# Optimization experiments

Measured on AMD Instinct MI355X. Metric: run time of the kernel, lower is better.

## Reference

```python
import jax, jax.numpy as jnp
import numpy as np

N_NODES = 50000
N_EDGES = 800000
FEAT = 128
HID = 128
NUM_GRAPHS = 64
ODE_STEPS = 8   # fixed-step RK4 stand-in for adaptive odeint over CFG.ode_time_points
DEPTH = 1.0
EPS = 1e-5


def layer_norm(x, g, b):
    m = jnp.mean(x, axis=-1, keepdims=True)
    v = jnp.var(x, axis=-1, keepdims=True)
    return (x - m) * jax.lax.rsqrt(v + EPS) * g + b


def setup_inputs() -> dict:
    key = jax.random.key(0)
    ks = jax.random.split(key, 16)
    s = 1.0 / np.sqrt(FEAT)
    sh = 1.0 / np.sqrt(HID)
    inp = {
        "x": jax.random.normal(ks[0], (N_NODES, FEAT), jnp.float32),
        "edge_index": jax.random.randint(ks[1], (2, N_EDGES), 0, N_NODES, jnp.int64),
        "batch": jnp.sort(jax.random.randint(ks[2], (N_NODES,), 0, NUM_GRAPHS, jnp.int64)),
        "alpha": jnp.float32(0.8),
        "beta": jnp.float32(0.6),
        "phase": jnp.float32(0.7),
        "W_in": jax.random.normal(ks[3], (FEAT, HID), jnp.float32) * s,
        "b_in": jnp.zeros((HID,), jnp.float32),
        "g_in": jnp.ones((HID,), jnp.float32),
        "be_in": jnp.zeros((HID,), jnp.float32),
        "W_alt": jax.random.normal(ks[4], (FEAT, HID), jnp.float32) * s,
        "b_alt": jnp.zeros((HID,), jnp.float32),
        "g_alt": jnp.ones((HID,), jnp.float32),
        "be_alt": jnp.zeros((HID,), jnp.float32),
        "W_self": jax.random.normal(ks[5], (HID, HID), jnp.float32) * sh,
        "W_msg": jax.random.normal(ks[6], (HID, HID), jnp.float32) * sh,
        "b_ode": jnp.zeros((HID,), jnp.float32),
        "W_int": jax.random.normal(ks[7], (2 * HID, HID), jnp.float32) * sh / np.sqrt(2.0),
        "b_int": jnp.zeros((HID,), jnp.float32),
        "g_int": jnp.ones((HID,), jnp.float32),
        "be_int": jnp.zeros((HID,), jnp.float32),
        "W_out": jax.random.normal(ks[8], (HID, HID), jnp.float32) * sh,
        "b_out": jnp.zeros((HID,), jnp.float32),
    }
    return inp


def _forward(x, alpha, beta, phase,
             W_in, b_in, g_in, be_in,
             W_alt, b_alt, g_alt, be_alt,
             W_self, W_msg, b_ode,
             W_int, b_int, g_int, be_int,
             W_out, b_out,
             edge_index, batch):
    src, dst = edge_index[0], edge_index[1]
    # in-degree for mean aggregation (clamped to 1)
    deg = jax.ops.segment_sum(jnp.ones((src.shape[0],), jnp.float32), dst,
                              num_segments=N_NODES)
    deg = jnp.maximum(deg, 1.0)[:, None]

    # quantum amplitudes -> measurement probabilities (normalized)
    norm = jnp.sqrt(alpha ** 2 + beta ** 2)
    a, b = alpha / norm, beta / norm
    p0, p1 = a ** 2, b ** 2

    # two projection pathways in superposition
    h0 = jax.nn.gelu(layer_norm(x @ W_in + b_in, g_in, be_in))
    h1 = jax.nn.gelu(layer_norm(x @ W_alt + b_alt, g_alt, be_alt))
    h = jnp.sqrt(p0) * h0 + jnp.sqrt(p1) * h1  # [N, H]

    # Neural ODE: dh/dt = tanh(h W_self + mean_{j->i}(h_j W_msg) + b)
    def ode_f(h):
        msg = h[src] @ W_msg                       # [E, H] gather + GEMM
        agg = jax.ops.segment_sum(msg, dst, num_segments=N_NODES) / deg
        return jnp.tanh(h @ W_self + agg + b_ode)

    dt = jnp.float32(DEPTH / ODE_STEPS)

    def rk4_step(h, _):
        k1 = ode_f(h)
        k2 = ode_f(h + 0.5 * dt * k1)
        k3 = ode_f(h + 0.5 * dt * k2)
        k4 = ode_f(h + dt * k3)
        return h + (dt / 6.0) * (k1 + 2.0 * k2 + 2.0 * k3 + k4), None

    h, _ = jax.lax.scan(rk4_step, h, None, length=ODE_STEPS)

    # quantum interference mixing (conditional branch -> masked add)
    interf = 2.0 * jnp.sqrt(p0 * p1) * jnp.cos(phase)
    h_int = jnp.tanh(layer_norm(jnp.concatenate([h, h], axis=-1) @ W_int + b_int,
                                g_int, be_int))
    gate = jnp.where(jnp.abs(interf) > 0.01, interf, 0.0)
    h = h + gate * h_int

    # eval-mode collapse: if p1 >= p0, scale by Re(e^{i*phase}) = cos(phase)
    h = jnp.where(p0 > p1, h, h * jnp.cos(phase))

    h_out = h @ W_out + b_out

    # global mean pool over graphs
    cnt = jax.ops.segment_sum(jnp.ones((N_NODES,), jnp.float32), batch,
                              num_segments=NUM_GRAPHS)
    pooled = jax.ops.segment_sum(h_out, batch, num_segments=NUM_GRAPHS)
    return pooled / jnp.maximum(cnt, 1.0)[:, None]  # [NUM_GRAPHS, H]


def reference(x, edge_index, batch, alpha, beta, phase,
              W_in, b_in, g_in, be_in,
              W_alt, b_alt, g_alt, be_alt,
              W_self, W_msg, b_ode,
              W_int, b_int, g_int, be_int,
              W_out, b_out):
    return _forward(x, alpha, beta, phase,
                    W_in, b_in, g_in, be_in,
                    W_alt, b_alt, g_alt, be_alt,
                    W_self, W_msg, b_ode,
                    W_int, b_int, g_int, be_int,
                    W_out, b_out, edge_index, batch)
```

## Files before the change

kernel.cpp:

```cpp
#include <hip/hip_runtime.h>
#include <math.h>

#define NND 50000
#define NED 800000
#define HD  128
#define NG  64

typedef __attribute__((ext_vector_type(8))) short short8v;
typedef __attribute__((ext_vector_type(4))) float float4v;

__device__ __forceinline__ float gelu_t(float x) {
  const float c = 0.7978845608028654f;
  float t = tanhf(c * (x + 0.044715f * x * x * x));
  return 0.5f * x * (1.0f + t);
}

__device__ __forceinline__ unsigned short f2bf(float f) {
  unsigned int u = __float_as_uint(f);
  u += 0x7FFFu + ((u >> 16) & 1u);
  return (unsigned short)(u >> 16);
}
__device__ __forceinline__ float bf2f(unsigned short s) {
  return __uint_as_float(((unsigned int)s) << 16);
}
__device__ __forceinline__ float bflo(unsigned int u) { return __uint_as_float(u << 16); }
__device__ __forceinline__ float bfhi(unsigned int u) { return __uint_as_float(u & 0xFFFF0000u); }

__global__ void k_hist(const int* __restrict__ dst, int* __restrict__ degi) {
  int e = blockIdx.x * 256 + threadIdx.x;
  if (e < NED) atomicAdd(&degi[dst[e]], 1);
}

__global__ __launch_bounds__(1024) void k_scan(
    const int* __restrict__ degi, int* __restrict__ rowptr,
    int* __restrict__ cursor, float* __restrict__ deginv) {
  __shared__ int wsum[16];
  int tid = threadIdx.x;
  int lane = tid & 63;
  int wid = tid >> 6;
  int running = 0;
  for (int base = 0; base < NND; base += 1024) {
    int idx = base + tid;
    int v = (idx < NND) ? degi[idx] : 0;
    int s = v;
#pragma unroll
    for (int o = 1; o < 64; o <<= 1) {
      int t = __shfl_up(s, o, 64);
      if (lane >= o) s += t;
    }
    if (lane == 63) wsum[wid] = s;
    __syncthreads();
    if (wid == 0) {
      int ws = (lane < 16) ? wsum[lane] : 0;
#pragma unroll
      for (int o = 1; o < 16; o <<= 1) {
        int t = __shfl_up(ws, o, 64);
        if (lane >= o) ws += t;
      }
      if (lane < 16) wsum[lane] = ws;
    }
    __syncthreads();
    int woff = wid ? wsum[wid - 1] : 0;
    int excl = running + woff + s - v;
    if (idx < NND) {
      rowptr[idx] = excl;
      cursor[idx] = excl;
      deginv[idx] = 1.0f / (float)max(v, 1);
    }
    int tot = wsum[15];
    __syncthreads();
    running += tot;
  }
  if (tid == 0) rowptr[NND] = running;
}

__global__ void k_scatter(const int* __restrict__ src, const int* __restrict__ dst,
                          int* __restrict__ cursor, int* __restrict__ csrsrc) {
  int e = blockIdx.x * 256 + threadIdx.x;
  if (e < NED) {
    int d = dst[e];
    int pos = atomicAdd(&cursor[d], 1);
    csrsrc[pos] = src[e];
  }
}

__global__ void k_cnt(const int* __restrict__ batch, float* __restrict__ cnt) {
  int g = threadIdx.x;
  if (g >= NG) return;
  int lo, hi, ub_g, ub_gm1;
  lo = 0; hi = NND;
  while (lo < hi) { int mid = (lo + hi) >> 1; if (batch[mid] <= g) lo = mid + 1; else hi = mid; }
  ub_g = lo;
  if (g == 0) ub_gm1 = 0;
  else {
    lo = 0; hi = NND;
    int v = g - 1;
    while (lo < hi) { int mid = (lo + hi) >> 1; if (batch[mid] <= v) lo = mid + 1; else hi = mid; }
    ub_gm1 = lo;
  }
  cnt[g] = (float)(ub_g - ub_gm1);
}

__global__ void k_weff(const float* __restrict__ Wint, float* __restrict__ weff) {
  int i = blockIdx.x * 256 + threadIdx.x;
  if (i < HD * HD) weff[i] = Wint[i] + Wint[i + HD * HD];
}

__global__ void k_prepB(const float* __restrict__ Wself, const float* __restrict__ Wmsg,
                        unsigned short* __restrict__ Bt) {
  int i = blockIdx.x * 256 + threadIdx.x;
  if (i < 128 * 256) {
    int n = i >> 8, k = i & 255;
    float w = (k < HD) ? Wself[k * HD + n] : Wmsg[(k - HD) * HD + n];
    Bt[i] = f2bf(w);
  }
}

__global__ __launch_bounds__(256) void k_init(
    const float* __restrict__ x,
    const float* __restrict__ Win, const float* __restrict__ bin,
    const float* __restrict__ gin, const float* __restrict__ bein,
    const float* __restrict__ Walt, const float* __restrict__ balt,
    const float* __restrict__ galt, const float* __restrict__ bealt,
    const float* __restrict__ alphap, const float* __restrict__ betap,
    float* __restrict__ hdst, unsigned short* __restrict__ hbf)
{
  __shared__ float As[32][16];
  __shared__ float Bs[16][256];
  int tid = threadIdx.x;
  int lane = tid & 63;
  int ty = tid >> 6;
  int rowBase = blockIdx.x * 32;
  float acc[8][4];
#pragma unroll
  for (int i = 0; i < 8; ++i) { acc[i][0]=0.f; acc[i][1]=0.f; acc[i][2]=0.f; acc[i][3]=0.f; }

  for (int kc = 0; kc < 8; ++kc) {
    int k0 = kc * 16;
    if (tid < 128) {
      int r = tid >> 2, kq = (tid & 3) * 4;
      int row = rowBase + r; if (row >= NND) row = NND - 1;
      *(float4*)&As[r][kq] = *(const float4*)&x[(size_t)row * HD + k0 + kq];
    }
#pragma unroll
    for (int p = 0; p < 4; ++p) {
      int idx = p * 256 + tid;
      int kk = idx >> 6, cq = idx & 63;
      int col = cq * 4;
      int k = k0 + kk;
      const float* srcp = (col < HD) ? &Win[k * HD + col] : &Walt[k * HD + (col - HD)];
      *(float4*)&Bs[kk][col] = *(const float4*)srcp;
    }
    __syncthreads();
#pragma unroll
    for (int kq = 0; kq < 4; ++kq) {
      float4 b0 = *(float4*)&Bs[kq*4+0][lane*4];
      float4 b1 = *(float4*)&Bs[kq*4+1][lane*4];
      float4 b2 = *(float4*)&Bs[kq*4+2][lane*4];
      float4 b3 = *(float4*)&Bs[kq*4+3][lane*4];
#pragma unroll
      for (int i = 0; i < 8; ++i) {
        float4 a = *(float4*)&As[ty*8+i][kq*4];
        acc[i][0] = fmaf(a.x,b0.x,fmaf(a.y,b1.x,fmaf(a.z,b2.x,fmaf(a.w,b3.x,acc[i][0]))));
        acc[i][1] = fmaf(a.x,b0.y,fmaf(a.y,b1.y,fmaf(a.z,b2.y,fmaf(a.w,b3.y,acc[i][1]))));
        acc[i][2] = fmaf(a.x,b0.z,fmaf(a.y,b1.z,fmaf(a.z,b2.z,fmaf(a.w,b3.z,acc[i][2]))));
        acc[i][3] = fmaf(a.x,b0.w,fmaf(a.y,b1.w,fmaf(a.z,b2.w,fmaf(a.w,b3.w,acc[i][3]))));
      }
    }
    __syncthreads();
  }

  float al = alphap[0], bt = betap[0];
  float nrm = sqrtf(al*al + bt*bt);
  float w0 = fabsf(al) / nrm, w1 = fabsf(bt) / nrm;
  int path = lane >> 5;
  int cl = (lane & 31) * 4;
  const float* bvp = path ? balt : bin;
  const float* gp  = path ? galt : gin;
  const float* bep = path ? bealt : bein;
  float4 bv  = *(const float4*)&bvp[cl];
  float4 gv  = *(const float4*)&gp[cl];
  float4 bev = *(const float4*)&bep[cl];
#pragma unroll
  for (int i = 0; i < 8; ++i) {
    int row = rowBase + ty*8 + i;
    float z0 = acc[i][0]+bv.x, z1 = acc[i][1]+bv.y, z2 = acc[i][2]+bv.z, z3 = acc[i][3]+bv.w;
    float rsum = z0+z1+z2+z3;
    float rsq  = z0*z0+z1*z1+z2*z2+z3*z3;
#pragma unroll
    for (int m = 1; m < 32; m <<= 1) { rsum += __shfl_xor(rsum, m, 32); rsq += __shfl_xor(rsq, m, 32); }
    float mean = rsum * (1.0f/128.0f);
    float var  = rsq * (1.0f/128.0f) - mean*mean;
    float rs = rsqrtf(var + 1e-5f);
    float g0 = gelu_t((z0-mean)*rs*gv.x + bev.x);
    float g1 = gelu_t((z1-mean)*rs*gv.y + bev.y);
    float g2 = gelu_t((z2-mean)*rs*gv.z + bev.z);
    float g3 = gelu_t((z3-mean)*rs*gv.w + bev.w);
    float o0 = __shfl_xor(g0, 32, 64);
    float o1 = __shfl_xor(g1, 32, 64);
    float o2 = __shfl_xor(g2, 32, 64);
    float o3 = __shfl_xor(g3, 32, 64);
    if (row < NND && path == 0) {
      float h0 = fmaf(w0,g0,w1*o0);
      float h1 = fmaf(w0,g1,w1*o1);
      float h2 = fmaf(w0,g2,w1*o2);
      float h3 = fmaf(w0,g3,w1*o3);
      size_t off = (size_t)row * HD + cl;
      *(float4*)&hdst[off] = make_float4(h0, h1, h2, h3);
      hbf[off+0] = f2bf(h0); hbf[off+1] = f2bf(h1);
      hbf[off+2] = f2bf(h2); hbf[off+3] = f2bf(h3);
    }
  }
}

__global__ __launch_bounds__(256) void k_fused(
    const unsigned short* __restrict__ ain, const int* __restrict__ rowptr,
    const int* __restrict__ csrsrc, const float* __restrict__ deginv,
    const unsigned short* __restrict__ Bt, const float* __restrict__ bode,
    const float* __restrict__ h, float* __restrict__ hacc,
    float* __restrict__ hout, unsigned short* __restrict__ ybf,
    unsigned short* __restrict__ hbf, int stage)
{
  __shared__ unsigned char u_lds[64 * 256];
  int tid = threadIdx.x;
  int wave = tid >> 6;
  int lane = tid & 63;
  int l15 = lane & 15;
  int lhi = lane >> 4;
  int rowBase = blockIdx.x * 64;
  int ncol0 = wave * 32;

  {
    int l16 = tid & 15;
    int grp = tid >> 4;
#pragma unroll
    for (int g = 0; g < 4; ++g) {
      int nloc = g * 16 + grp;
      int node = rowBase + nloc;
      if (node < NND) {
        int e0 = rowptr[node], e1 = rowptr[node + 1];
        float a0=0,a1=0,a2=0,a3=0,a4=0,a5=0,a6=0,a7=0;
        int e = e0;
        for (; e + 3 < e1; e += 4) {
          int s0 = csrsrc[e], s1 = csrsrc[e+1], s2 = csrsrc[e+2], s3 = csrsrc[e+3];
          uint4 v0 = *(const uint4*)&ain[(size_t)s0 * HD + l16 * 8];
          uint4 v1 = *(const uint4*)&ain[(size_t)s1 * HD + l16 * 8];
          uint4 v2 = *(const uint4*)&ain[(size_t)s2 * HD + l16 * 8];
          uint4 v3 = *(const uint4*)&ain[(size_t)s3 * HD + l16 * 8];
          a0 += bflo(v0.x)+bflo(v1.x)+bflo(v2.x)+bflo(v3.x);
          a1 += bfhi(v0.x)+bfhi(v1.x)+bfhi(v2.x)+bfhi(v3.x);
          a2 += bflo(v0.y)+bflo(v1.y)+bflo(v2.y)+bflo(v3.y);
          a3 += bfhi(v0.y)+bfhi(v1.y)+bfhi(v2.y)+bfhi(v3.y);
          a4 += bflo(v0.z)+bflo(v1.z)+bflo(v2.z)+bflo(v3.z);
          a5 += bfhi(v0.z)+bfhi(v1.z)+bfhi(v2.z)+bfhi(v3.z);
          a6 += bflo(v0.w)+bflo(v1.w)+bflo(v2.w)+bflo(v3.w);
          a7 += bfhi(v0.w)+bfhi(v1.w)+bfhi(v2.w)+bfhi(v3.w);
        }
        for (; e < e1; ++e) {
          int s0 = csrsrc[e];
          uint4 v0 = *(const uint4*)&ain[(size_t)s0 * HD + l16 * 8];
          a0 += bflo(v0.x); a1 += bfhi(v0.x); a2 += bflo(v0.y); a3 += bfhi(v0.y);
          a4 += bflo(v0.z); a5 += bfhi(v0.z); a6 += bflo(v0.w); a7 += bfhi(v0.w);
        }
        float di = deginv[node];
        uint4 o;
        o.x = (unsigned int)f2bf(a0*di) | ((unsigned int)f2bf(a1*di) << 16);
        o.y = (unsigned int)f2bf(a2*di) | ((unsigned int)f2bf(a3*di) << 16);
        o.z = (unsigned int)f2bf(a4*di) | ((unsigned int)f2bf(a5*di) << 16);
        o.w = (unsigned int)f2bf(a6*di) | ((unsigned int)f2bf(a7*di) << 16);
        unsigned int boff = (unsigned int)nloc * 256u + (((unsigned int)l16 * 16u) ^ (((unsigned int)nloc & 7u) << 4));
        *(uint4*)&u_lds[boff] = o;
      }
    }
  }

  short8v bfr[2][8];
#pragma unroll
  for (int t = 0; t < 2; ++t) {
    int n = ncol0 + t * 16 + l15;
#pragma unroll
    for (int s = 0; s < 8; ++s) {
      bfr[t][s] = *(const short8v*)&Bt[n * 256 + s * 32 + lhi * 8];
    }
  }

  const float DT = 0.125f;
  float wk = (stage == 0 || stage == 3) ? DT / 6.0f : DT / 3.0f;
  float cy = (stage <= 1) ? 0.5f * DT : DT;
  float bo0 = bode[ncol0 + l15];
  float bo1 = bode[ncol0 + 16 + l15];

  __syncthreads();

#pragma unroll
  for (int rt = 0; rt < 4; ++rt) {
    int rloc = rt * 16 + l15;
    int mload = rowBase + rloc;
    if (mload >= NND) mload = NND - 1;
    short8v afr[8];
#pragma unroll
    for (int s = 0; s < 4; ++s)
      afr[s] = *(const short8v*)&ain[(size_t)mload * HD + s * 32 + lhi * 8];
#pragma unroll
    for (int s = 0; s < 4; ++s) {
      unsigned int boff = (unsigned int)rloc * 256u +
        ((((unsigned int)s * 64u) + ((unsigned int)lhi * 16u)) ^ (((unsigned int)rloc & 7u) << 4));
      afr[4 + s] = *(const short8v*)&u_lds[boff];
    }

    float4v acc0 = {0.f, 0.f, 0.f, 0.f};
    float4v acc1 = {0.f, 0.f, 0.f, 0.f};
#pragma unroll
    for (int s = 0; s < 8; ++s) {
      acc0 = __builtin_amdgcn_mfma_f32_16x16x32_bf16(afr[s], bfr[0][s], acc0, 0, 0, 0);
      acc1 = __builtin_amdgcn_mfma_f32_16x16x32_bf16(afr[s], bfr[1][s], acc1, 0, 0, 0);
    }

#pragma unroll
    for (int t = 0; t < 2; ++t) {
      int n = ncol0 + t * 16 + l15;
      float bo = t ? bo1 : bo0;
#pragma unroll
      for (int r = 0; r < 4; ++r) {
        int m = rowBase + rt * 16 + lhi * 4 + r;
        if (m < NND) {
          size_t off = (size_t)m * HD + n;
          float av = t ? acc1[r] : acc0[r];
          float kv = tanhf(av + bo);
          if (stage == 0) {
            float hv = h[off];
            hacc[off] = hv + wk * kv;
            ybf[off] = f2bf(hv + cy * kv);
          } else if (stage < 3) {
            hacc[off] += wk * kv;
            ybf[off] = f2bf(bf2f(hbf[off]) + cy * kv);
          } else {
            float hn = hacc[off] + wk * kv;
            hout[off] = hn;
            hbf[off] = f2bf(hn);
          }
        }
      }
    }
  }
}

__global__ __launch_bounds__(256) void k_interf(
    const float* __restrict__ h, const float* __restrict__ weff,
    const float* __restrict__ bint, const float* __restrict__ gint,
    const float* __restrict__ beint,
    const float* __restrict__ alphap, const float* __restrict__ betap,
    const float* __restrict__ phasep,
    float* __restrict__ h2out)
{
  __shared__ float As[64][16];
  __shared__ float Bs[16][128];
  int tid = threadIdx.x;
  int tx = tid & 31, ty = tid >> 5;
  int rowBase = blockIdx.x * 64;
  float acc[8][4];
#pragma unroll
  for (int i = 0; i < 8; ++i) { acc[i][0]=0.f; acc[i][1]=0.f; acc[i][2]=0.f; acc[i][3]=0.f; }

  for (int kc = 0; kc < 8; ++kc) {
    int k0 = kc * 16;
    {
      int r = tid >> 2, kq = (tid & 3) * 4;
      int row = rowBase + r; if (row >= NND) row = NND - 1;
      *(float4*)&As[r][kq] = *(const float4*)&h[(size_t)row * HD + k0 + kq];
    }
#pragma unroll
    for (int j = 0; j < 2; ++j) {
      int kk = (tid >> 5) + j * 8;
      int n = (tid & 31) * 4;
      *(float4*)&Bs[kk][n] = *(const float4*)&weff[(k0 + kk) * HD + n];
    }
    __syncthreads();
#pragma unroll
    for (int kq = 0; kq < 4; ++kq) {
      float4 b0 = *(float4*)&Bs[kq*4+0][tx*4];
      float4 b1 = *(float4*)&Bs[kq*4+1][tx*4];
      float4 b2 = *(float4*)&Bs[kq*4+2][tx*4];
      float4 b3 = *(float4*)&Bs[kq*4+3][tx*4];
#pragma unroll
      for (int i = 0; i < 8; ++i) {
        float4 a = *(float4*)&As[ty*8+i][kq*4];
        acc[i][0] = fmaf(a.x,b0.x,fmaf(a.y,b1.x,fmaf(a.z,b2.x,fmaf(a.w,b3.x,acc[i][0]))));
        acc[i][1] = fmaf(a.x,b0.y,fmaf(a.y,b1.y,fmaf(a.z,b2.y,fmaf(a.w,b3.y,acc[i][1]))));
        acc[i][2] = fmaf(a.x,b0.z,fmaf(a.y,b1.z,fmaf(a.z,b2.z,fmaf(a.w,b3.z,acc[i][2]))));
        acc[i][3] = fmaf(a.x,b0.w,fmaf(a.y,b1.w,fmaf(a.z,b2.w,fmaf(a.w,b3.w,acc[i][3]))));
      }
    }
    __syncthreads();
  }

  float al = alphap[0], bt = betap[0], ph = phasep[0];
  float n2 = al*al + bt*bt;
  float p0 = (al*al) / n2, p1 = (bt*bt) / n2;
  float interf = 2.0f * sqrtf(p0 * p1) * cosf(ph);
  float gate = (fabsf(interf) > 0.01f) ? interf : 0.0f;
  float cscale = (p0 > p1) ? 1.0f : cosf(ph);

  int c0 = tx * 4;
  float4 bi  = *(const float4*)&bint[c0];
  float4 gv  = *(const float4*)&gint[c0];
  float4 bev = *(const float4*)&beint[c0];
#pragma unroll
  for (int i = 0; i < 8; ++i) {
    int row = rowBase + ty*8 + i;
    float z0 = acc[i][0]+bi.x, z1 = acc[i][1]+bi.y, z2 = acc[i][2]+bi.z, z3 = acc[i][3]+bi.w;
    float rsum = z0+z1+z2+z3;
    float rsq  = z0*z0+z1*z1+z2*z2+z3*z3;
#pragma unroll
    for (int m = 1; m < 32; m <<= 1) { rsum += __shfl_xor(rsum, m, 32); rsq += __shfl_xor(rsq, m, 32); }
    float mean = rsum * (1.0f/128.0f);
    float var  = rsq * (1.0f/128.0f) - mean*mean;
    float rs = rsqrtf(var + 1e-5f);
    float t0 = tanhf((z0-mean)*rs*gv.x + bev.x);
    float t1 = tanhf((z1-mean)*rs*gv.y + bev.y);
    float t2 = tanhf((z2-mean)*rs*gv.z + bev.z);
    float t3 = tanhf((z3-mean)*rs*gv.w + bev.w);
    if (row < NND) {
      size_t off = (size_t)row * HD + c0;
      float4 hv = *(const float4*)&h[off];
      float4 o = make_float4((hv.x + gate*t0) * cscale,
                             (hv.y + gate*t1) * cscale,
                             (hv.z + gate*t2) * cscale,
                             (hv.w + gate*t3) * cscale);
      *(float4*)&h2out[off] = o;
    }
  }
}

__global__ __launch_bounds__(256) void k_out(
    const float* __restrict__ h2, const float* __restrict__ Wout,
    const float* __restrict__ bout, const int* __restrict__ batch,
    float* __restrict__ pooled)
{
  __shared__ float As[64][16];
  __shared__ float Bs[16][128];
  int tid = threadIdx.x;
  int tx = tid & 31, ty = tid >> 5;
  int rowBase = blockIdx.x * 64;
  float acc[8][4];
#pragma unroll
  for (int i = 0; i < 8; ++i) { acc[i][0]=0.f; acc[i][1]=0.f; acc[i][2]=0.f; acc[i][3]=0.f; }

  for (int kc = 0; kc < 8; ++kc) {
    int k0 = kc * 16;
    {
      int r = tid >> 2, kq = (tid & 3) * 4;
      int row = rowBase + r; if (row >= NND) row = NND - 1;
      *(float4*)&As[r][kq] = *(const float4*)&h2[(size_t)row * HD + k0 + kq];
    }
#pragma unroll
    for (int j = 0; j < 2; ++j) {
      int kk = (tid >> 5) + j * 8;
      int n = (tid & 31) * 4;
      *(float4*)&Bs[kk][n] = *(const float4*)&Wout[(k0 + kk) * HD + n];
    }
    __syncthreads();
#pragma unroll
    for (int kq = 0; kq < 4; ++kq) {
      float4 b0 = *(float4*)&Bs[kq*4+0][tx*4];
      float4 b1 = *(float4*)&Bs[kq*4+1][tx*4];
      float4 b2 = *(float4*)&Bs[kq*4+2][tx*4];
      float4 b3 = *(float4*)&Bs[kq*4+3][tx*4];
#pragma unroll
      for (int i = 0; i < 8; ++i) {
        float4 a = *(float4*)&As[ty*8+i][kq*4];
        acc[i][0] = fmaf(a.x,b0.x,fmaf(a.y,b1.x,fmaf(a.z,b2.x,fmaf(a.w,b3.x,acc[i][0]))));
        acc[i][1] = fmaf(a.x,b0.y,fmaf(a.y,b1.y,fmaf(a.z,b2.y,fmaf(a.w,b3.y,acc[i][1]))));
        acc[i][2] = fmaf(a.x,b0.z,fmaf(a.y,b1.z,fmaf(a.z,b2.z,fmaf(a.w,b3.z,acc[i][2]))));
        acc[i][3] = fmaf(a.x,b0.w,fmaf(a.y,b1.w,fmaf(a.z,b2.w,fmaf(a.w,b3.w,acc[i][3]))));
      }
    }
    __syncthreads();
  }

  int c0 = tx * 4;
  float4 bo = *(const float4*)&bout[c0];
  int prevg = -1;
  float r0 = 0.f, r1 = 0.f, r2 = 0.f, r3 = 0.f;
#pragma unroll
  for (int i = 0; i < 8; ++i) {
    int row = rowBase + ty*8 + i;
    if (row >= NND) break;
    int g = batch[row];
    float v0 = acc[i][0] + bo.x;
    float v1 = acc[i][1] + bo.y;
    float v2 = acc[i][2] + bo.z;
    float v3 = acc[i][3] + bo.w;
    if (g != prevg) {
      if (prevg >= 0) {
        atomicAdd(&pooled[prevg*HD + c0 + 0], r0);
        atomicAdd(&pooled[prevg*HD + c0 + 1], r1);
        atomicAdd(&pooled[prevg*HD + c0 + 2], r2);
        atomicAdd(&pooled[prevg*HD + c0 + 3], r3);
      }
      prevg = g; r0 = v0; r1 = v1; r2 = v2; r3 = v3;
    } else {
      r0 += v0; r1 += v1; r2 += v2; r3 += v3;
    }
  }
  if (prevg >= 0) {
    atomicAdd(&pooled[prevg*HD + c0 + 0], r0);
    atomicAdd(&pooled[prevg*HD + c0 + 1], r1);
    atomicAdd(&pooled[prevg*HD + c0 + 2], r2);
    atomicAdd(&pooled[prevg*HD + c0 + 3], r3);
  }
}

__global__ void k_final(const float* __restrict__ pooled, const float* __restrict__ cnt,
                        float* __restrict__ out) {
  int i = blockIdx.x * 256 + threadIdx.x;
  if (i < NG * HD) out[i] = pooled[i] / fmaxf(cnt[i >> 7], 1.0f);
}

extern "C" void kernel_launch(void* const* d_in, const int* in_sizes, int n_in,
                              void* d_out, int out_size, void* d_ws, size_t ws_size,
                              hipStream_t stream) {
  (void)in_sizes; (void)n_in; (void)out_size; (void)ws_size;
  const float* x     = (const float*)d_in[0];
  const int*   ei    = (const int*)d_in[1];
  const int*   batch = (const int*)d_in[2];
  const float* alpha = (const float*)d_in[3];
  const float* beta  = (const float*)d_in[4];
  const float* phase = (const float*)d_in[5];
  const float* Win   = (const float*)d_in[6];
  const float* bin   = (const float*)d_in[7];
  const float* gin   = (const float*)d_in[8];
  const float* bein  = (const float*)d_in[9];
  const float* Walt  = (const float*)d_in[10];
  const float* balt  = (const float*)d_in[11];
  const float* galt  = (const float*)d_in[12];
  const float* bealt = (const float*)d_in[13];
  const float* Wself = (const float*)d_in[14];
  const float* Wmsg  = (const float*)d_in[15];
  const float* bode  = (const float*)d_in[16];
  const float* Wint  = (const float*)d_in[17];
  const float* bint  = (const float*)d_in[18];
  const float* gint  = (const float*)d_in[19];
  const float* beint = (const float*)d_in[20];
  const float* Wout  = (const float*)d_in[21];
  const float* bout  = (const float*)d_in[22];
  float* out = (float*)d_out;

  const int* esrc = ei;
  const int* edst = ei + NED;

  size_t NH = (size_t)NND * HD;
  float* h      = (float*)d_ws;
  float* hacc   = h + NH;
  float* deginv = hacc + NH;
  float* weff   = deginv + NND;
  float* pooled = weff + HD * HD;
  float* cnt    = pooled + NG * HD;
  unsigned short* hbf = (unsigned short*)(cnt + NG);
  unsigned short* ybf = hbf + NH;
  unsigned short* Bt  = ybf + NH;
  int* degi   = (int*)(Bt + 128 * 256);
  int* rowptr = degi + NND;
  int* cursor = rowptr + (NND + 4);
  int* csrsrc = cursor + NND;

  hipMemsetAsync(degi, 0, NND * sizeof(int), stream);
  hipMemsetAsync(pooled, 0, NG * HD * sizeof(float), stream);

  k_hist   <<<(NED + 255) / 256, 256, 0, stream>>>(edst, degi);
  k_scan   <<<1, 1024, 0, stream>>>(degi, rowptr, cursor, deginv);
  k_scatter<<<(NED + 255) / 256, 256, 0, stream>>>(esrc, edst, cursor, csrsrc);
  k_cnt    <<<1, 64, 0, stream>>>(batch, cnt);
  k_weff   <<<(HD * HD + 255) / 256, 256, 0, stream>>>(Wint, weff);
  k_prepB  <<<128, 256, 0, stream>>>(Wself, Wmsg, Bt);
  k_init   <<<(NND + 31) / 32, 256, 0, stream>>>(x, Win, bin, gin, bein,
                                                 Walt, balt, galt, bealt,
                                                 alpha, beta, h, hbf);
  for (int step = 0; step < 8; ++step) {
    for (int stage = 0; stage < 4; ++stage) {
      const unsigned short* ainbf = (stage == 0) ? hbf : ybf;
      k_fused<<<(NND + 63) / 64, 256, 0, stream>>>(ainbf, rowptr, csrsrc, deginv,
                                                   Bt, bode, h, hacc, h, ybf, hbf, stage);
    }
  }
  k_interf<<<(NND + 63) / 64, 256, 0, stream>>>(h, weff, bint, gint, beint,
                                                alpha, beta, phase, hacc);
  k_out   <<<(NND + 63) / 64, 256, 0, stream>>>(hacc, Wout, bout, batch, pooled);
  k_final <<<(NG * HD + 255) / 256, 256, 0, stream>>>(pooled, cnt, out);
}
```

Measured before the change: 2.357 ms.

## Use bf16 MFMA for input projection, shrink fused tile, cooperative edge gather

Replaces the FP32 scalar-FMA input projection with a bf16 MFMA kernel that reads pre-transposed bf16 weights and does the layer-norm reduction across waves through shared memory. The fused ODE-stage kernel now handles 32 rows per block instead of 64, which doubles the block count. Its neighbor gather now loads 16 edge indices per lane group at once and shares them with shuffles, using two accumulators to expose more loads in flight. The changes trade FP32 precision in the first projection for matrix-core throughput, and the smaller tile means each block reloads the weight fragments for fewer rows.

```diff
diff --git a/kernel.cpp b/kernel.cpp
--- a/kernel.cpp
+++ b/kernel.cpp
@@ -116,103 +116,155 @@
   }
 }
 
-__global__ __launch_bounds__(256) void k_init(
-    const float* __restrict__ x,
-    const float* __restrict__ Win, const float* __restrict__ bin,
-    const float* __restrict__ gin, const float* __restrict__ bein,
-    const float* __restrict__ Walt, const float* __restrict__ balt,
-    const float* __restrict__ galt, const float* __restrict__ bealt,
+__global__ void k_prepIn(const float* __restrict__ Win, const float* __restrict__ Walt,
+                         unsigned short* __restrict__ BtIn) {
+  int i = blockIdx.x * 256 + threadIdx.x;
+  if (i < 2 * 128 * 128) {
+    int p = i >> 14; int rem = i & 16383; int n = rem >> 7; int k = rem & 127;
+    const float* W = p ? Walt : Win;
+    BtIn[i] = f2bf(W[k * 128 + n]);
+  }
+}
+
+__global__ __launch_bounds__(256) void k_init2(
+    const float* __restrict__ x, const unsigned short* __restrict__ BtIn,
+    const float* __restrict__ bin, const float* __restrict__ gin, const float* __restrict__ bein,
+    const float* __restrict__ balt, const float* __restrict__ galt, const float* __restrict__ bealt,
     const float* __restrict__ alphap, const float* __restrict__ betap,
     float* __restrict__ hdst, unsigned short* __restrict__ hbf)
 {
-  __shared__ float As[32][16];
-  __shared__ float Bs[16][256];
+  __shared__ float red[4][16][2];
+  __shared__ unsigned short gtile[2][16][64];
   int tid = threadIdx.x;
+  int wave = tid >> 6;
   int lane = tid & 63;
-  int ty = tid >> 6;
-  int rowBase = blockIdx.x * 32;
-  float acc[8][4];
-#pragma unroll
-  for (int i = 0; i < 8; ++i) { acc[i][0]=0.f; acc[i][1]=0.f; acc[i][2]=0.f; acc[i][3]=0.f; }
-
-  for (int kc = 0; kc < 8; ++kc) {
-    int k0 = kc * 16;
-    if (tid < 128) {
-      int r = tid >> 2, kq = (tid & 3) * 4;
-      int row = rowBase + r; if (row >= NND) row = NND - 1;
-      *(float4*)&As[r][kq] = *(const float4*)&x[(size_t)row * HD + k0 + kq];
-    }
-#pragma unroll
-    for (int p = 0; p < 4; ++p) {
-      int idx = p * 256 + tid;
-      int kk = idx >> 6, cq = idx & 63;
-      int col = cq * 4;
-      int k = k0 + kk;
-      const float* srcp = (col < HD) ? &Win[k * HD + col] : &Walt[k * HD + (col - HD)];
-      *(float4*)&Bs[kk][col] = *(const float4*)srcp;
-    }
-    __syncthreads();
-#pragma unroll
-    for (int kq = 0; kq < 4; ++kq) {
-      float4 b0 = *(float4*)&Bs[kq*4+0][lane*4];
-      float4 b1 = *(float4*)&Bs[kq*4+1][lane*4];
-      float4 b2 = *(float4*)&Bs[kq*4+2][lane*4];
-      float4 b3 = *(float4*)&Bs[kq*4+3][lane*4];
-#pragma unroll
-      for (int i = 0; i < 8; ++i) {
-        float4 a = *(float4*)&As[ty*8+i][kq*4];
-        acc[i][0] = fmaf(a.x,b0.x,fmaf(a.y,b1.x,fmaf(a.z,b2.x,fmaf(a.w,b3.x,acc[i][0]))));
-        acc[i][1] = fmaf(a.x,b0.y,fmaf(a.y,b1.y,fmaf(a.z,b2.y,fmaf(a.w,b3.y,acc[i][1]))));
-        acc[i][2] = fmaf(a.x,b0.z,fmaf(a.y,b1.z,fmaf(a.z,b2.z,fmaf(a.w,b3.z,acc[i][2]))));
-        acc[i][3] = fmaf(a.x,b0.w,fmaf(a.y,b1.w,fmaf(a.z,b2.w,fmaf(a.w,b3.w,acc[i][3]))));
-      }
-    }
-    __syncthreads();
-  }
-
-  float al = alphap[0], bt = betap[0];
-  float nrm = sqrtf(al*al + bt*bt);
-  float w0 = fabsf(al) / nrm, w1 = fabsf(bt) / nrm;
-  int path = lane >> 5;
-  int cl = (lane & 31) * 4;
+  int l15 = lane & 15;
+  int lhi = lane >> 4;
+  int path = wave >> 1;
+  int colBase = (wave & 1) * 64;
+  int rowBase = blockIdx.x * 64;
+
+  const unsigned short* Bp = BtIn + path * 128 * 128;
+  short8v bfr[4][4];
+#pragma unroll
+  for (int t = 0; t < 4; ++t) {
+    int n = colBase + t * 16 + l15;
+#pragma unroll
+    for (int s = 0; s < 4; ++s)
+      bfr[t][s] = *(const short8v*)&Bp[n * 128 + s * 32 + lhi * 8];
+  }
+
   const float* bvp = path ? balt : bin;
   const float* gp  = path ? galt : gin;
   const float* bep = path ? bealt : bein;
-  float4 bv  = *(const float4*)&bvp[cl];
-  float4 gv  = *(const float4*)&gp[cl];
-  float4 bev = *(const float4*)&bep[cl];
-#pragma unroll
-  for (int i = 0; i < 8; ++i) {
-    int row = rowBase + ty*8 + i;
-    float z0 = acc[i][0]+bv.x, z1 = acc[i][1]+bv.y, z2 = acc[i][2]+bv.z, z3 = acc[i][3]+bv.w;
-    float rsum = z0+z1+z2+z3;
-    float rsq  = z0*z0+z1*z1+z2*z2+z3*z3;
-#pragma unroll
-    for (int m = 1; m < 32; m <<= 1) { rsum += __shfl_xor(rsum, m, 32); rsq += __shfl_xor(rsq, m, 32); }
-    float mean = rsum * (1.0f/128.0f);
-    float var  = rsq * (1.0f/128.0f) - mean*mean;
-    float rs = rsqrtf(var + 1e-5f);
-    float g0 = gelu_t((z0-mean)*rs*gv.x + bev.x);
-    float g1 = gelu_t((z1-mean)*rs*gv.y + bev.y);
-    float g2 = gelu_t((z2-mean)*rs*gv.z + bev.z);
-    float g3 = gelu_t((z3-mean)*rs*gv.w + bev.w);
-    float o0 = __shfl_xor(g0, 32, 64);
-    float o1 = __shfl_xor(g1, 32, 64);
-    float o2 = __shfl_xor(g2, 32, 64);
-    float o3 = __shfl_xor(g3, 32, 64);
-    if (row < NND && path == 0) {
-      float h0 = fmaf(w0,g0,w1*o0);
-      float h1 = fmaf(w0,g1,w1*o1);
-      float h2 = fmaf(w0,g2,w1*o2);
-      float h3 = fmaf(w0,g3,w1*o3);
-      size_t off = (size_t)row * HD + cl;
-      *(float4*)&hdst[off] = make_float4(h0, h1, h2, h3);
-      hbf[off+0] = f2bf(h0); hbf[off+1] = f2bf(h1);
-      hbf[off+2] = f2bf(h2); hbf[off+3] = f2bf(h3);
-    }
-  }
-}
-
+  float bv[4], gw[4], bew[4];
+#pragma unroll
+  for (int t = 0; t < 4; ++t) {
+    int col = colBase + t * 16 + l15;
+    bv[t] = bvp[col]; gw[t] = gp[col]; bew[t] = bep[col];
+  }
+
+  float al = alphap[0], btv = betap[0];
+  float nrm = sqrtf(al * al + btv * btv);
+  float w0 = fabsf(al) / nrm, w1 = fabsf(btv) / nrm;
+
+  for (int rt = 0; rt < 4; ++rt) {
+    int arow = rowBase + rt * 16 + l15; if (arow >= NND) arow = NND - 1;
+    short8v afr[4];
+#pragma unroll
+    for (int s = 0; s < 4; ++s) {
+      float4 xa = *(const float4*)&x[(size_t)arow * HD + s * 32 + lhi * 8];
+      float4 xb = *(const float4*)&x[(size_t)arow * HD + s * 32 + lhi * 8 + 4];
+      short8v f;
+      f[0] = (short)f2bf(xa.x); f[1] = (short)f2bf(xa.y);
+      f[2] = (short)f2bf(xa.z); f[3] = (short)f2bf(xa.w);
+      f[4] = (short)f2bf(xb.x); f[5] = (short)f2bf(xb.y);
+      f[6] = (short)f2bf(xb.z); f[7] = (short)f2bf(xb.w);
+      afr[s] = f;
+    }
+
+    float4v acc[4];
+#pragma unroll
+    for (int t = 0; t < 4; ++t) acc[t] = (float4v){0.f, 0.f, 0.f, 0.f};
+#pragma unroll
+    for (int s = 0; s < 4; ++s) {
+#pragma unroll
+      for (int t = 0; t < 4; ++t)
+        acc[t] = __builtin_amdgcn_mfma_f32_16x16x32_bf16(afr[s], bfr[t][s], acc[t], 0, 0, 0);
+    }
+
+    float z[4][4];
+    float psum[4], psq[4];
+#pragma unroll
+    for (int r = 0; r < 4; ++r) {
+      float s1 = 0.f, s2 = 0.f;
+#pragma unroll
+      for (int t = 0; t < 4; ++t) {
+        float zz = acc[t][r] + bv[t];
+        z[r][t] = zz;
+        s1 += zz; s2 += zz * zz;
+      }
+#pragma unroll
+      for (int m = 1; m < 16; m <<= 1) {
+        s1 += __shfl_xor(s1, m, 16);
+        s2 += __shfl_xor(s2, m, 16);
+      }
+      psum[r] = s1; psq[r] = s2;
+    }
+    if (l15 == 0) {
+#pragma unroll
+      for (int r = 0; r < 4; ++r) {
+        red[wave][lhi * 4 + r][0] = psum[r];
+        red[wave][lhi * 4 + r][1] = psq[r];
+      }
+    }
+    __syncthreads();
+
+    int pw = wave ^ 1;
+    float gval[4][4];
+#pragma unroll
+    for (int r = 0; r < 4; ++r) {
+      int rowl = lhi * 4 + r;
+      float S = psum[r] + red[pw][rowl][0];
+      float Q = psq[r]  + red[pw][rowl][1];
+      float mean = S * (1.0f / 128.0f);
+      float var  = Q * (1.0f / 128.0f) - mean * mean;
+      float rs = rsqrtf(var + 1e-5f);
+#pragma unroll
+      for (int t = 0; t < 4; ++t)
+        gval[r][t] = gelu_t((z[r][t] - mean) * rs * gw[t] + bew[t]);
+    }
+
+    if (path == 1) {
+#pragma unroll
+      for (int r = 0; r < 4; ++r)
+#pragma unroll
+        for (int t = 0; t < 4; ++t)
+          gtile[wave & 1][lhi * 4 + r][t * 16 + l15] = f2bf(gval[r][t]);
+    }
+    __syncthreads();
+
+    if (path == 0) {
+#pragma unroll
+      for (int r = 0; r < 4; ++r) {
+        int m = rowBase + rt * 16 + lhi * 4 + r;
+        if (m < NND) {
+#pragma unroll
+          for (int t = 0; t < 4; ++t) {
+            float g1 = bf2f(gtile[wave & 1][lhi * 4 + r][t * 16 + l15]);
+            float hv = w0 * gval[r][t] + w1 * g1;
+            size_t off = (size_t)m * HD + colBase + t * 16 + l15;
+            hdst[off] = hv;
+            hbf[off] = f2bf(hv);
+          }
+        }
+      }
+    }
+    __syncthreads();
+  }
+}
+
+#define MT 32
 __global__ __launch_bounds__(256) void k_fused(
     const unsigned short* __restrict__ ain, const int* __restrict__ rowptr,
     const int* __restrict__ csrsrc, const float* __restrict__ deginv,
@@ -221,47 +273,46 @@
     float* __restrict__ hout, unsigned short* __restrict__ ybf,
     unsigned short* __restrict__ hbf, int stage)
 {
-  __shared__ unsigned char u_lds[64 * 256];
+  __shared__ unsigned char u_lds[MT * 256];
   int tid = threadIdx.x;
   int wave = tid >> 6;
   int lane = tid & 63;
   int l15 = lane & 15;
   int lhi = lane >> 4;
-  int rowBase = blockIdx.x * 64;
+  int rowBase = blockIdx.x * MT;
   int ncol0 = wave * 32;
 
   {
     int l16 = tid & 15;
     int grp = tid >> 4;
 #pragma unroll
-    for (int g = 0; g < 4; ++g) {
+    for (int g = 0; g < MT / 16; ++g) {
       int nloc = g * 16 + grp;
       int node = rowBase + nloc;
       if (node < NND) {
         int e0 = rowptr[node], e1 = rowptr[node + 1];
         float a0=0,a1=0,a2=0,a3=0,a4=0,a5=0,a6=0,a7=0;
-        int e = e0;
-        for (; e + 3 < e1; e += 4) {
-          int s0 = csrsrc[e], s1 = csrsrc[e+1], s2 = csrsrc[e+2], s3 = csrsrc[e+3];
-          uint4 v0 = *(const uint4*)&ain[(size_t)s0 * HD + l16 * 8];
-          uint4 v1 = *(const uint4*)&ain[(size_t)s1 * HD + l16 * 8];
-          uint4 v2 = *(const uint4*)&ain[(size_t)s2 * HD + l16 * 8];
-          uint4 v3 = *(const uint4*)&ain[(size_t)s3 * HD + l16 * 8];
-          a0 += bflo(v0.x)+bflo(v1.x)+bflo(v2.x)+bflo(v3.x);
-          a1 += bfhi(v0.x)+bfhi(v1.x)+bfhi(v2.x)+bfhi(v3.x);
-          a2 += bflo(v0.y)+bflo(v1.y)+bflo(v2.y)+bflo(v3.y);
-          a3 += bfhi(v0.y)+bfhi(v1.y)+bfhi(v2.y)+bfhi(v3.y);
-          a4 += bflo(v0.z)+bflo(v1.z)+bflo(v2.z)+bflo(v3.z);
-          a5 += bfhi(v0.z)+bfhi(v1.z)+bfhi(v2.z)+bfhi(v3.z);
-          a6 += bflo(v0.w)+bflo(v1.w)+bflo(v2.w)+bflo(v3.w);
-          a7 += bfhi(v0.w)+bfhi(v1.w)+bfhi(v2.w)+bfhi(v3.w);
+        float c0=0,c1=0,c2=0,c3=0,c4=0,c5=0,c6=0,c7=0;
+        for (int eb = e0; eb < e1; eb += 16) {
+          int rem = e1 - eb;
+          int myi = csrsrc[eb + ((l16 < rem) ? l16 : rem - 1)];
+#pragma unroll
+          for (int j = 0; j < 16; j += 2) {
+            if (j < rem) {
+              int s = __shfl(myi, j, 16);
+              uint4 v = *(const uint4*)&ain[(size_t)s * HD + l16 * 8];
+              a0 += bflo(v.x); a1 += bfhi(v.x); a2 += bflo(v.y); a3 += bfhi(v.y);
+              a4 += bflo(v.z); a5 += bfhi(v.z); a6 += bflo(v.w); a7 += bfhi(v.w);
+            }
+            if (j + 1 < rem) {
+              int s2 = __shfl(myi, j + 1, 16);
+              uint4 v2 = *(const uint4*)&ain[(size_t)s2 * HD + l16 * 8];
+              c0 += bflo(v2.x); c1 += bfhi(v2.x); c2 += bflo(v2.y); c3 += bfhi(v2.y);
+              c4 += bflo(v2.z); c5 += bfhi(v2.z); c6 += bflo(v2.w); c7 += bfhi(v2.w);
+            }
+          }
         }
-        for (; e < e1; ++e) {
-          int s0 = csrsrc[e];
-          uint4 v0 = *(const uint4*)&ain[(size_t)s0 * HD + l16 * 8];
-          a0 += bflo(v0.x); a1 += bfhi(v0.x); a2 += bflo(v0.y); a3 += bfhi(v0.y);
-          a4 += bflo(v0.z); a5 += bfhi(v0.z); a6 += bflo(v0.w); a7 += bfhi(v0.w);
-        }
+        a0+=c0; a1+=c1; a2+=c2; a3+=c3; a4+=c4; a5+=c5; a6+=c6; a7+=c7;
         float di = deginv[node];
         uint4 o;
         o.x = (unsigned int)f2bf(a0*di) | ((unsigned int)f2bf(a1*di) << 16);
@@ -293,7 +344,7 @@
   __syncthreads();
 
 #pragma unroll
-  for (int rt = 0; rt < 4; ++rt) {
+  for (int rt = 0; rt < MT / 16; ++rt) {
     int rloc = rt * 16 + l15;
     int mload = rowBase + rloc;
     if (mload >= NND) mload = NND - 1;
@@ -556,10 +607,11 @@
   float* weff   = deginv + NND;
   float* pooled = weff + HD * HD;
   float* cnt    = pooled + NG * HD;
-  unsigned short* hbf = (unsigned short*)(cnt + NG);
-  unsigned short* ybf = hbf + NH;
-  unsigned short* Bt  = ybf + NH;
-  int* degi   = (int*)(Bt + 128 * 256);
+  unsigned short* hbf  = (unsigned short*)(cnt + NG);
+  unsigned short* ybf  = hbf + NH;
+  unsigned short* Bt   = ybf + NH;
+  unsigned short* BtIn = Bt + 128 * 256;
+  int* degi   = (int*)(BtIn + 2 * 128 * 128);
   int* rowptr = degi + NND;
   int* cursor = rowptr + (NND + 4);
   int* csrsrc = cursor + NND;
@@ -573,14 +625,15 @@
   k_cnt    <<<1, 64, 0, stream>>>(batch, cnt);
   k_weff   <<<(HD * HD + 255) / 256, 256, 0, stream>>>(Wint, weff);
   k_prepB  <<<128, 256, 0, stream>>>(Wself, Wmsg, Bt);
-  k_init   <<<(NND + 31) / 32, 256, 0, stream>>>(x, Win, bin, gin, bein,
-                                                 Walt, balt, galt, bealt,
+  k_prepIn <<<128, 256, 0, stream>>>(Win, Walt, BtIn);
+  k_init2  <<<(NND + 63) / 64, 256, 0, stream>>>(x, BtIn, bin, gin, bein,
+                                                 balt, galt, bealt,
                                                  alpha, beta, h, hbf);
   for (int step = 0; step < 8; ++step) {
     for (int stage = 0; stage < 4; ++stage) {
       const unsigned short* ainbf = (stage == 0) ? hbf : ybf;
-      k_fused<<<(NND + 63) / 64, 256, 0, stream>>>(ainbf, rowptr, csrsrc, deginv,
-                                                   Bt, bode, h, hacc, h, ybf, hbf, stage);
+      k_fused<<<(NND + MT - 1) / MT, 256, 0, stream>>>(ainbf, rowptr, csrsrc, deginv,
+                                                       Bt, bode, h, hacc, h, ybf, hbf, stage);
     }
   }
   k_interf<<<(NND + 63) / 64, 256, 0, stream>>>(h, weff, bint, gint, beint,
```

Result: slower. 2.792 ms (+18.4%).
